# Performance work log

Hardware: AMD Instinct MI355X
Metric: run time of the kernel (lower is better)

The kernel has to match this reference:

```python
import jax, jax.numpy as jnp
import numpy as np


def conv2d(x, w, b, pad=1):
    y = jax.lax.conv_general_dilated(x, w, (1, 1), [(pad, pad), (pad, pad)],
                                     dimension_numbers=('NCHW', 'OIHW', 'NCHW'))
    return y + b[None, :, None, None]


def deform_conv2d(x, offsets, w, b, groups=8, pad=1):
    # torchvision-style deformable conv: offsets [B, 2*G*K, H, W] laid out as
    # (g, k, (dy, dx)); input channels split into G offset groups; zero padding
    # outside the image for bilinear sampling.
    B, C, H, W = x.shape
    kh, kw = w.shape[2], w.shape[3]
    K = kh * kw
    cpg = C // groups
    off = offsets.reshape(B, groups, K, 2, H, W)
    dy, dx = off[:, :, :, 0], off[:, :, :, 1]  # [B,G,K,H,W]
    ky, kx = jnp.meshgrid(jnp.arange(kh), jnp.arange(kw), indexing='ij')
    ky = ky.reshape(K).astype(x.dtype)
    kx = kx.reshape(K).astype(x.dtype)
    ygrid = jnp.arange(H, dtype=x.dtype)
    xgrid = jnp.arange(W, dtype=x.dtype)
    # absolute sampling positions [B,G,K,H,W]
    py = ygrid[None, None, None, :, None] + (ky - pad)[None, None, :, None, None] + dy
    px = xgrid[None, None, None, None, :] + (kx - pad)[None, None, :, None, None] + dx
    y0 = jnp.floor(py)
    x0 = jnp.floor(px)
    wy = py - y0  # frac weights [B,G,K,H,W]
    wx = px - x0
    y0i = y0.astype(jnp.int32)
    x0i = x0.astype(jnp.int32)
    xg = x.reshape(B, groups, cpg, H * W)

    def gather(yc, xc):
        valid = ((yc >= 0) & (yc < H) & (xc >= 0) & (xc < W)).astype(x.dtype)
        idx = jnp.clip(yc, 0, H - 1) * W + jnp.clip(xc, 0, W - 1)
        idx = jnp.broadcast_to(idx.reshape(B, groups, 1, K * H * W),
                               (B, groups, cpg, K * H * W))
        v = jnp.take_along_axis(xg, idx, axis=3).reshape(B, groups, cpg, K, H, W)
        return v * valid[:, :, None]

    v00 = gather(y0i, x0i)
    v01 = gather(y0i, x0i + 1)
    v10 = gather(y0i + 1, x0i)
    v11 = gather(y0i + 1, x0i + 1)
    wy_ = wy[:, :, None]  # [B,G,1,K,H,W]
    wx_ = wx[:, :, None]
    sampled = (v00 * (1 - wy_) * (1 - wx_) + v01 * (1 - wy_) * wx_
               + v10 * wy_ * (1 - wx_) + v11 * wy_ * wx_)
    sampled = sampled.reshape(B, C, K, H, W)
    out = jnp.einsum('bckhw,ock->bohw', sampled, w.reshape(w.shape[0], C, K))
    return out + b[None, :, None, None]


def dab(feat, aux_in, aux_w, aux_b, fw1, fb1, fw2, fb2, se_w1, se_b1, se_w2, se_b2):
    # Adaptive fusion block: project aux (128->64), concat, conv-relu-conv body,
    # SE channel attention (reduction=2), residual add onto feat.
    aux = jax.nn.relu(conv2d(aux_in, aux_w, aux_b))
    x = jnp.concatenate([feat, aux], axis=1)  # [B,128,H,W]
    x = jax.nn.relu(conv2d(x, fw1, fb1))      # 128->64
    x = conv2d(x, fw2, fb2)                   # 64->64
    g = jnp.mean(x, axis=(2, 3))              # [B,64]
    a = jax.nn.sigmoid(jax.nn.relu(g @ se_w1.T + se_b1) @ se_w2.T + se_b2)
    return feat + x * a[:, :, None, None]


def setup_inputs() -> dict:
    key = jax.random.key(0)
    ks = jax.random.split(key, 16)
    B, H, W = 4, 192, 192

    def p(k, shape, s=0.05):
        return jax.random.normal(k, shape, jnp.float32) * s

    return {
        'mv': jax.random.normal(ks[0], (B, 128, H, W), jnp.float32),
        'ref_feature': jax.random.normal(ks[1], (B, 64, H, W), jnp.float32),
        'head_w': p(ks[2], (144, 128, 3, 3)), 'head_b': jnp.zeros((144,), jnp.float32),
        'dcn_w': p(ks[3], (64, 64, 3, 3)), 'dcn_b': jnp.zeros((64,), jnp.float32),
        'c1w1': p(ks[4], (128, 64, 3, 3)), 'c1b1': jnp.zeros((128,), jnp.float32),
        'c1w2': p(ks[5], (128, 128, 3, 3)), 'c1b2': jnp.zeros((128,), jnp.float32),
        'aux_w': p(ks[6], (64, 128, 3, 3)), 'aux_b': jnp.zeros((64,), jnp.float32),
        'fw1': p(ks[7], (64, 128, 3, 3)), 'fb1': jnp.zeros((64,), jnp.float32),
        'fw2': p(ks[8], (64, 64, 3, 3)), 'fb2': jnp.zeros((64,), jnp.float32),
        'se_w1': p(ks[9], (32, 64)), 'se_b1': jnp.zeros((32,), jnp.float32),
        'se_w2': p(ks[10], (64, 32)), 'se_b2': jnp.zeros((64,), jnp.float32),
    }


def reference(mv, ref_feature, head_w, head_b, dcn_w, dcn_b, c1w1, c1b1, c1w2, c1b2,
              aux_w, aux_b, fw1, fb1, fw2, fb2, se_w1, se_b1, se_w2, se_b2):
    offsets = conv2d(mv, head_w, head_b)                       # [B,144,H,W]
    def_feat = jax.nn.relu(deform_conv2d(ref_feature, offsets, dcn_w, dcn_b))
    aux_in = jax.nn.relu(conv2d(jax.nn.relu(conv2d(ref_feature, c1w1, c1b1)),
                                c1w2, c1b2))                   # convs1: 64->128->128
    return dab(def_feat, aux_in, aux_w, aux_b, fw1, fb1, fw2, fb2,
               se_w1, se_b1, se_w2, se_b2)
```

## Files before the change

kernel.cpp:

```cpp
#include <hip/hip_runtime.h>
#include <math.h>

#define HH 192
#define WW 192
#define HWSZ (HH*WW)
#define BB 4

typedef __attribute__((ext_vector_type(8))) short bf16x8;
typedef __attribute__((ext_vector_type(4))) float f32x4;

__device__ __forceinline__ unsigned short f2bf(float f) {
    unsigned int u = __float_as_uint(f);
    u = (u + 0x7FFFu + ((u >> 16) & 1u)) >> 16;
    return (unsigned short)u;
}
__device__ __forceinline__ float bf2f(unsigned short s) {
    return __uint_as_float(((unsigned int)s) << 16);
}

__global__ void prep_all(
    const float* __restrict__ head_w, const float* __restrict__ c1w1,
    const float* __restrict__ c1w2,   const float* __restrict__ aux_w,
    const float* __restrict__ fw1,    const float* __restrict__ fw2,
    const float* __restrict__ dcn_w,
    unsigned short* __restrict__ wb_head, unsigned short* __restrict__ wb_c1w1,
    unsigned short* __restrict__ wb_c1w2, unsigned short* __restrict__ wb_aux,
    unsigned short* __restrict__ wb_fw1,  unsigned short* __restrict__ wb_fw2,
    unsigned short* __restrict__ wdefb2)
{
    int idx = blockIdx.x * 256 + threadIdx.x;
    const float* w; unsigned short* wb; int cout, cin;
    if (idx < 165888)                 { w = head_w; wb = wb_head; cout = 144; cin = 128; }
    else if ((idx -= 165888) < 73728) { w = c1w1;   wb = wb_c1w1; cout = 128; cin = 64;  }
    else if ((idx -= 73728) < 147456) { w = c1w2;   wb = wb_c1w2; cout = 128; cin = 128; }
    else if ((idx -= 147456) < 73728) { w = aux_w;  wb = wb_aux;  cout = 64;  cin = 128; }
    else if ((idx -= 73728) < 73728)  { w = fw1;    wb = wb_fw1;  cout = 64;  cin = 128; }
    else if ((idx -= 73728) < 36864)  { w = fw2;    wb = wb_fw2;  cout = 64;  cin = 64;  }
    else if ((idx -= 36864) < 36864) {
        int o = idx / 576, rem = idx % 576;
        int c = rem / 9, k = rem - c * 9;
        int K = k * 64 + c;
        wdefb2[((size_t)((K >> 5) * 64 + o)) * 32 + (K & 31)] = f2bf(dcn_w[idx]);
        return;
    } else return;
    int o = idx / (cin * 9);
    int rem = idx - o * cin * 9;
    int c = rem / 9;
    int t = rem - c * 9;
    int nch = cin >> 5;
    wb[((t * nch + (c >> 5)) * cout + o) * 32 + (c & 31)] = f2bf(w[idx]);
}

__global__ __launch_bounds__(256) void transpose_all(
    const float* __restrict__ mv, const float* __restrict__ ref,
    unsigned short* __restrict__ mvb, unsigned short* __restrict__ refb,
    unsigned short* __restrict__ refb8)
{
    __shared__ float tile[32][68];
    const int tid = threadIdx.x;
    int bz = blockIdx.z;
    const float* in; unsigned short* outb;
    bool isRef = (bz >= 16);
    int bzr = isRef ? bz - 16 : bz;
    if (isRef) { in = ref; outb = refb; }
    else       { in = mv;  outb = mvb;  }
    const int y = blockIdx.y;
    const int x0 = blockIdx.x * 64;
#pragma unroll
    for (int it = 0; it < 2; ++it) {
        int u = tid + it * 256;
        int c = u >> 4, q = u & 15;
        float4 v = *(const float4*)(in + (((size_t)bzr * 32 + c) * HH + y) * WW + x0 + q * 4);
        *(float4*)&tile[c][q * 4] = v;
    }
    __syncthreads();
    const int pxl = tid >> 2, c8 = tid & 3;
    bf16x8 ov;
#pragma unroll
    for (int j = 0; j < 8; ++j) ov[j] = (short)f2bf(tile[c8 * 8 + j][pxl]);
    *(bf16x8*)(outb + (((size_t)bzr * HH + y) * WW + x0 + pxl) * 32 + c8 * 8) = ov;
    if (isRef) {
        *(bf16x8*)(refb8 + ((size_t)(bzr * 4 + c8) * HWSZ + (size_t)y * WW + x0 + pxl) * 8) = ov;
    }
}

template<int CIN, int COUT_TILE, bool RELU, int EPI>
__global__ __launch_bounds__(256, 3) void conv3x3_v10(
    const unsigned short* __restrict__ in, const unsigned short* __restrict__ wb,
    const float* __restrict__ bias, void* __restrict__ outp,
    int cTot, int ocBase, int nOc, int coutFull, int nPerXcd)
{
    constexpr int NCH = CIN / 32;
    constexpr int NOC = COUT_TILE / 16;
    constexpr int WGR = 36 * COUT_TILE;
    __shared__ __align__(16) unsigned short sx[6 * 72 * 32];
    __shared__ __align__(16) unsigned short sw[288 * COUT_TILE];

    const int tid = threadIdx.x;
    const int d = blockIdx.x;
    const int w = (d & 7) * nPerXcd + (d >> 3);
    const int ocT = (w % nOc) * COUT_TILE;
    int t = w / nOc;
    const int x0 = (t % 3) * 64; t /= 3;
    const int y0 = (t % 48) * 4;
    const int b  = t / 48;
    const int wv = tid >> 6, lane = tid & 63;
    const int l15 = lane & 15, kg = lane >> 4;

    f32x4 acc[NOC][4];
#pragma unroll
    for (int oc = 0; oc < NOC; ++oc)
#pragma unroll
        for (int s = 0; s < 4; ++s) acc[oc][s] = (f32x4){0.f, 0.f, 0.f, 0.f};

    for (int ch = 0; ch < NCH; ++ch) {
#pragma unroll
        for (int it = 0; it < 7; ++it) {
            int u = tid + it * 256;
            if (u < 1728) {
                int r = u / 288;
                int rem = u - r * 288;
                int px = rem >> 2, c8 = rem & 3;
                int yin = y0 - 1 + r;
                int gx  = x0 - 4 + px;
                bf16x8 v = {0,0,0,0,0,0,0,0};
                if (yin >= 0 && yin < HH && gx >= 0 && gx < WW)
                    v = *(const bf16x8*)(in + (((size_t)(b * NCH + ch) * HH + yin) * WW + gx) * 32 + c8 * 8);
                *(bf16x8*)&sx[(r * 72 + px) * 32 + ((c8 ^ ((px >> 1) & 3)) << 3)] = v;
            }
        }
#pragma unroll
        for (int it = 0; it < 7; ++it) {
            int u = tid + it * 256;
            if (u < WGR) {
                int tap = u / (4 * COUT_TILE);
                int rem = u - tap * 4 * COUT_TILE;
                int kgi = rem / COUT_TILE;
                int row = rem - kgi * COUT_TILE;
                bf16x8 v = *(const bf16x8*)(wb
                    + ((size_t)((tap * NCH + ch) * coutFull) + ocT + row) * 32 + kgi * 8);
                *(bf16x8*)&sw[((tap * 4 + kgi) * COUT_TILE + row) * 8] = v;
            }
        }
        __syncthreads();
#pragma unroll
        for (int ky = 0; ky < 3; ++ky) {
#pragma unroll
            for (int kx = 0; kx < 3; ++kx) {
                const int r = wv + ky;
                const int tap = ky * 3 + kx;
                bf16x8 bf[4];
#pragma unroll
                for (int s = 0; s < 4; ++s) {
                    int p = s * 16 + l15 + kx + 3;
                    bf[s] = *(const bf16x8*)&sx[(r * 72 + p) * 32 + ((kg ^ ((p >> 1) & 3)) << 3)];
                }
#pragma unroll
                for (int oc = 0; oc < NOC; ++oc) {
                    bf16x8 a = *(const bf16x8*)&sw[((tap * 4 + kg) * COUT_TILE + oc * 16 + l15) * 8];
#pragma unroll
                    for (int s = 0; s < 4; ++s)
                        acc[oc][s] = __builtin_amdgcn_mfma_f32_16x16x32_bf16(a, bf[s], acc[oc][s], 0, 0, 0);
                }
            }
        }
        __syncthreads();
    }
    const int y = y0 + wv;
    if (EPI == 1) {
        float* out = (float*)outp;
#pragma unroll
        for (int oc = 0; oc < NOC; ++oc)
#pragma unroll
            for (int s = 0; s < 4; ++s) {
                int xo = x0 + s * 16 + l15;
#pragma unroll
                for (int j = 0; j < 4; ++j) {
                    int oL = ocT + oc * 16 + kg * 4 + j;
                    float rv = acc[oc][s][j] + bias[oL];
                    if (RELU) rv = fmaxf(rv, 0.f);
                    out[((size_t)(b * cTot + ocBase + oL) * HH + y) * WW + xo] = rv;
                }
            }
    } else if (EPI == 2) {
        unsigned short* out = (unsigned short*)outp;
#pragma unroll
        for (int oc = 0; oc < NOC; ++oc)
#pragma unroll
            for (int s = 0; s < 4; ++s) {
                int xo = x0 + s * 16 + l15;
#pragma unroll
                for (int j = 0; j < 4; ++j) {
                    int oL = ocT + oc * 16 + kg * 4 + j;
                    float rv = acc[oc][s][j] + bias[oL];
                    if (RELU) rv = fmaxf(rv, 0.f);
                    out[((size_t)(b * cTot + ocBase + oL) * HH + y) * WW + xo] = f2bf(rv);
                }
            }
    } else {
        unsigned short* out = (unsigned short*)outp;
#pragma unroll
        for (int oc = 0; oc < NOC; ++oc) {
            int oL = ocT + oc * 16 + kg * 4;
            int o0 = ocBase + oL;
#pragma unroll
            for (int s = 0; s < 4; ++s) {
                int xo = x0 + s * 16 + l15;
                ushort4 u;
                float r0 = acc[oc][s][0] + bias[oL + 0];
                float r1 = acc[oc][s][1] + bias[oL + 1];
                float r2 = acc[oc][s][2] + bias[oL + 2];
                float r3 = acc[oc][s][3] + bias[oL + 3];
                if (RELU) { r0 = fmaxf(r0,0.f); r1 = fmaxf(r1,0.f); r2 = fmaxf(r2,0.f); r3 = fmaxf(r3,0.f); }
                u.x = f2bf(r0); u.y = f2bf(r1); u.z = f2bf(r2); u.w = f2bf(r3);
                *(ushort4*)(out + ((((size_t)(b * cTot + (o0 >> 5)) * HH + y) * WW + xo) * 32) + (o0 & 31)) = u;
            }
        }
    }
}

__global__ __launch_bounds__(512, 4) void deform_v7(
    const unsigned short* __restrict__ xb8, const unsigned short* __restrict__ offb,
    const unsigned short* __restrict__ wdefb2, const float* __restrict__ bias,
    unsigned short* __restrict__ cat)
{
    __shared__ __align__(16) unsigned short smp[64 * 584];
    const int tid = threadIdx.x;
    const int b = blockIdx.z;
    int flat = blockIdx.x;
    int nf = (flat & 7) * 72 + (flat >> 3);
    const int pixbase = nf * 64;

    const int px = tid & 63, g = tid >> 6;
    const int pix = pixbase + px;
    const int y = pix / WW, x = pix - y * WW;

    const char* xgb = (const char*)(xb8 + (size_t)(b * 8 + g) * HWSZ * 8);
    const unsigned short* ob = offb + ((size_t)(b * 144 + g * 18)) * HWSZ + pix;

    float dyv[9], dxv[9];
#pragma unroll
    for (int k = 0; k < 9; ++k) {
        dyv[k] = bf2f(ob[(size_t)(2 * k) * HWSZ]);
        dxv[k] = bf2f(ob[(size_t)(2 * k + 1) * HWSZ]);
    }

    auto calc = [&](int k, int vo[4], float w4[4]) {
        float pyf = (float)(y + k / 3 - 1) + dyv[k];
        float pxf = (float)(x + k % 3 - 1) + dxv[k];
        float fy = floorf(pyf), fx = floorf(pxf);
        float wy = pyf - fy, wx = pxf - fx;
        int iy = (int)fy, ix = (int)fx;
        float w00 = (1.f - wy) * (1.f - wx), w01 = (1.f - wy) * wx;
        float w10 = wy * (1.f - wx),         w11 = wy * wx;
        bool y0v = (iy >= 0) && (iy < HH);
        bool y1v = (iy + 1 >= 0) && (iy + 1 < HH);
        bool x0v = (ix >= 0) && (ix < WW);
        bool x1v = (ix + 1 >= 0) && (ix + 1 < WW);
        if (!(y0v && x0v)) w00 = 0.f;
        if (!(y0v && x1v)) w01 = 0.f;
        if (!(y1v && x0v)) w10 = 0.f;
        if (!(y1v && x1v)) w11 = 0.f;
        int cy0 = min(max(iy, 0), HH - 1), cy1 = min(max(iy + 1, 0), HH - 1);
        int cx0 = min(max(ix, 0), WW - 1), cx1 = min(max(ix + 1, 0), WW - 1);
        vo[0] = (cy0 * WW + cx0) * 16;
        vo[1] = (cy0 * WW + cx1) * 16;
        vo[2] = (cy1 * WW + cx0) * 16;
        vo[3] = (cy1 * WW + cx1) * 16;
        w4[0] = w00; w4[1] = w01; w4[2] = w10; w4[3] = w11;
    };

    float wr[3][4];
    bf16x8 pf[2][4];
    {
        int vo[4]; calc(0, vo, wr[0]);
#pragma unroll
        for (int j = 0; j < 4; ++j) pf[0][j] = *(const bf16x8*)(xgb + vo[j]);
    }
    {
        int vo[4]; calc(1, vo, wr[1]);
#pragma unroll
        for (int j = 0; j < 4; ++j) pf[1][j] = *(const bf16x8*)(xgb + vo[j]);
    }
    unsigned short* so = smp + px * 584 + g * 8;
#pragma unroll
    for (int k = 0; k < 9; ++k) {
        bf16x8 nx0, nx1, nx2, nx3;
        if (k + 2 < 9) {
            int vo[4]; calc(k + 2, vo, wr[(k + 2) % 3]);
            nx0 = *(const bf16x8*)(xgb + vo[0]);
            nx1 = *(const bf16x8*)(xgb + vo[1]);
            nx2 = *(const bf16x8*)(xgb + vo[2]);
            nx3 = *(const bf16x8*)(xgb + vo[3]);
        }
        __builtin_amdgcn_sched_barrier(0);
        bf16x8 ov;
#pragma unroll
        for (int cc = 0; cc < 8; ++cc) {
            float s = bf2f((unsigned short)pf[k & 1][0][cc]) * wr[k % 3][0]
                    + bf2f((unsigned short)pf[k & 1][1][cc]) * wr[k % 3][1]
                    + bf2f((unsigned short)pf[k & 1][2][cc]) * wr[k % 3][2]
                    + bf2f((unsigned short)pf[k & 1][3][cc]) * wr[k % 3][3];
            ov[cc] = (short)f2bf(s);
        }
        *(bf16x8*)(so + k * 64) = ov;
        if (k + 2 < 9) { pf[k & 1][0] = nx0; pf[k & 1][1] = nx1; pf[k & 1][2] = nx2; pf[k & 1][3] = nx3; }
    }
    __syncthreads();
    const int wv = tid >> 6;
    const int lane = tid & 63, l15 = lane & 15, kg = lane >> 4;
    const int oc = wv >> 1, sp = (wv & 1) * 2;
    f32x4 acc0 = (f32x4){0.f, 0.f, 0.f, 0.f};
    f32x4 acc1 = (f32x4){0.f, 0.f, 0.f, 0.f};
    const unsigned short* arow = wdefb2 + ((size_t)(oc * 16 + l15)) * 32 + kg * 8;
#pragma unroll
    for (int ch = 0; ch < 18; ++ch) {
        bf16x8 b0 = *(const bf16x8*)&smp[(sp * 16 + l15) * 584 + ch * 32 + kg * 8];
        bf16x8 b1 = *(const bf16x8*)&smp[((sp + 1) * 16 + l15) * 584 + ch * 32 + kg * 8];
        bf16x8 a = *(const bf16x8*)(arow + (size_t)ch * 64 * 32);
        acc0 = __builtin_amdgcn_mfma_f32_16x16x32_bf16(a, b0, acc0, 0, 0, 0);
        acc1 = __builtin_amdgcn_mfma_f32_16x16x32_bf16(a, b1, acc1, 0, 0, 0);
    }
    const int o0 = oc * 16 + kg * 4;
#pragma unroll
    for (int s = 0; s < 2; ++s) {
        const f32x4& av = s ? acc1 : acc0;
        int pxo = pixbase + (sp + s) * 16 + l15;
        int yo = pxo / WW, xo = pxo - yo * WW;
        ushort4 u;
        u.x = f2bf(fmaxf(av[0] + bias[o0 + 0], 0.f));
        u.y = f2bf(fmaxf(av[1] + bias[o0 + 1], 0.f));
        u.z = f2bf(fmaxf(av[2] + bias[o0 + 2], 0.f));
        u.w = f2bf(fmaxf(av[3] + bias[o0 + 3], 0.f));
        *(ushort4*)(cat + ((((size_t)(b * 4 + (o0 >> 5)) * HH + yo) * WW + xo) * 32) + (o0 & 31)) = u;
    }
}

__global__ __launch_bounds__(256) void pool_kernel(const float* __restrict__ x, float* __restrict__ gout)
{
    int bc = blockIdx.x;
    const float* p = x + (size_t)bc * HWSZ;
    int tid = threadIdx.x;
    float s = 0.f;
    for (int i = tid * 4; i < HWSZ; i += 256 * 4) {
        float4 v = *reinterpret_cast<const float4*>(p + i);
        s += v.x + v.y + v.z + v.w;
    }
#pragma unroll
    for (int o = 32; o > 0; o >>= 1) s += __shfl_down(s, o, 64);
    __shared__ float red[4];
    if ((tid & 63) == 0) red[tid >> 6] = s;
    __syncthreads();
    if (tid == 0) gout[bc] = (red[0] + red[1] + red[2] + red[3]) * (1.f / (float)HWSZ);
}

__global__ __launch_bounds__(256) void se_kernel(
    const float* __restrict__ g, const float* __restrict__ w1, const float* __restrict__ b1,
    const float* __restrict__ w2, const float* __restrict__ b2, float* __restrict__ a)
{
    __shared__ float sg[BB * 64];
    __shared__ float sh[BB * 32];
    int tid = threadIdx.x;
    sg[tid] = g[tid];
    __syncthreads();
    if (tid < BB * 32) {
        int b = tid / 32, h = tid % 32;
        float s = b1[h];
        for (int c = 0; c < 64; ++c) s += sg[b * 64 + c] * w1[h * 64 + c];
        sh[b * 32 + h] = fmaxf(s, 0.f);
    }
    __syncthreads();
    {
        int b = tid / 64, o = tid % 64;
        float s = b2[o];
        for (int h = 0; h < 32; ++h) s += sh[b * 32 + h] * w2[o * 32 + h];
        a[tid] = 1.f / (1.f + expf(-s));
    }
}

__global__ __launch_bounds__(256) void final_v2(
    float* __restrict__ out, const unsigned short* __restrict__ catb, const float* __restrict__ a)
{
    const int VPC = HWSZ / 4;
    int v = blockIdx.x * 256 + threadIdx.x;
    int bc = v / VPC, within = v - bc * VPC;
    int b = bc >> 6, c = bc & 63;
    float av = a[bc];
    int pix = within * 4;
    int y = pix / WW, x = pix - y * WW;
    const unsigned short* dbase = catb
        + (((size_t)(b * 4 + (c >> 5)) * HH + y) * WW + x) * 32 + (c & 31);
    float4 xo = reinterpret_cast<float4*>(out)[v];
    float4 r;
    r.x = bf2f(dbase[0])  + xo.x * av;
    r.y = bf2f(dbase[32]) + xo.y * av;
    r.z = bf2f(dbase[64]) + xo.z * av;
    r.w = bf2f(dbase[96]) + xo.w * av;
    reinterpret_cast<float4*>(out)[v] = r;
}

extern "C" void kernel_launch(void* const* d_in, const int* in_sizes, int n_in,
                              void* d_out, int out_size, void* d_ws, size_t ws_size,
                              hipStream_t stream) {
    const float* mv     = (const float*)d_in[0];
    const float* ref    = (const float*)d_in[1];
    const float* head_w = (const float*)d_in[2];
    const float* head_b = (const float*)d_in[3];
    const float* dcn_w  = (const float*)d_in[4];
    const float* dcn_b  = (const float*)d_in[5];
    const float* c1w1   = (const float*)d_in[6];
    const float* c1b1   = (const float*)d_in[7];
    const float* c1w2   = (const float*)d_in[8];
    const float* c1b2   = (const float*)d_in[9];
    const float* aux_w  = (const float*)d_in[10];
    const float* aux_b  = (const float*)d_in[11];
    const float* fw1    = (const float*)d_in[12];
    const float* fb1    = (const float*)d_in[13];
    const float* fw2    = (const float*)d_in[14];
    const float* fb2    = (const float*)d_in[15];
    const float* se_w1  = (const float*)d_in[16];
    const float* se_b1  = (const float*)d_in[17];
    const float* se_w2  = (const float*)d_in[18];
    const float* se_b2  = (const float*)d_in[19];
    float* out = (float*)d_out;

    float* ws = (float*)d_ws;
    unsigned short* offb     = (unsigned short*)ws;
    unsigned short* mvb      = (unsigned short*)(ws + 21233664);
    unsigned short* refb     = (unsigned short*)(ws + 30670848);
    unsigned short* catb     = (unsigned short*)(ws + 35389440);
    unsigned short* r2b      = (unsigned short*)(ws + 44826624);
    unsigned short* wdefb2   = (unsigned short*)(ws + 54263808);
    unsigned short* wbb      = (unsigned short*)(ws + 54282240);
    unsigned short* refb8    = wbb + 571392;
    float* gbuf              = (float*)(refb8 + 9437184 + 16);
    float* abuf              = gbuf + 256;
    unsigned short* t1b      = (unsigned short*)ws;

    unsigned short* wb_head = wbb;
    unsigned short* wb_c1w1 = wb_head + 165888;
    unsigned short* wb_c1w2 = wb_c1w1 + 73728;
    unsigned short* wb_aux  = wb_c1w2 + 147456;
    unsigned short* wb_fw1  = wb_aux  + 73728;
    unsigned short* wb_fw2  = wb_fw1  + 73728;

    prep_all<<<2376, 256, 0, stream>>>(head_w, c1w1, c1w2, aux_w, fw1, fw2, dcn_w,
                                       wb_head, wb_c1w1, wb_c1w2, wb_aux, wb_fw1, wb_fw2, wdefb2);
    transpose_all<<<dim3(3, 192, 24), 256, 0, stream>>>(mv, ref, mvb, refb, refb8);

    conv3x3_v10<128, 48, false, 2><<<1728, 256, 0, stream>>>(
        mvb, wb_head, head_b, offb, 144, 0, 3, 144, 216);
    deform_v7<<<dim3(576, 1, BB), 512, 0, stream>>>(refb8, offb, wdefb2, dcn_b, catb);
    conv3x3_v10<64, 32, true, 0><<<2304, 256, 0, stream>>>(
        refb, wb_c1w1, c1b1, t1b, 4, 0, 4, 128, 288);
    conv3x3_v10<128, 32, true, 0><<<2304, 256, 0, stream>>>(
        t1b, wb_c1w2, c1b2, r2b, 4, 0, 4, 128, 288);
    conv3x3_v10<128, 32, true, 0><<<1152, 256, 0, stream>>>(
        r2b, wb_aux, aux_b, catb, 4, 64, 2, 64, 144);
    conv3x3_v10<128, 32, true, 0><<<1152, 256, 0, stream>>>(
        catb, wb_fw1, fb1, r2b, 2, 0, 2, 64, 144);
    conv3x3_v10<64, 32, false, 1><<<1152, 256, 0, stream>>>(
        r2b, wb_fw2, fb2, out, 64, 0, 2, 64, 144);
    pool_kernel<<<BB * 64, 256, 0, stream>>>(out, gbuf);
    se_kernel<<<1, 256, 0, stream>>>(gbuf, se_w1, se_b1, se_w2, se_b2, abuf);
    final_v2<<<9216, 256, 0, stream>>>(out, catb, abuf);
}
```

Before: 435.0 us.

## Keep last conv output in bf16 channel-blocked layout for pooling and final fuse

The final 3x3 conv now writes bf16 in the 32-channel-blocked layout into a reused workspace buffer, instead of fp32 NCHW into the output. A new pooling kernel reduces that bf16 buffer per 32-channel block, and the final SE-scale-plus-residual kernel reads it instead of re-reading fp32 output. The aim is to cut the fp32 write and two fp32 reads of the intermediate. In exchange, the pre-SE activations are rounded to bf16, and pooling now runs on only 8 blocks, which may underuse the GPU.

Measured after the change: 601.5 us. 38.3% more time.

```diff
diff --git a/kernel.cpp b/kernel.cpp
--- a/kernel.cpp
+++ b/kernel.cpp
@@ -336,22 +336,30 @@
     }
 }
 
-__global__ __launch_bounds__(256) void pool_kernel(const float* __restrict__ x, float* __restrict__ gout)
-{
-    int bc = blockIdx.x;
-    const float* p = x + (size_t)bc * HWSZ;
-    int tid = threadIdx.x;
-    float s = 0.f;
-    for (int i = tid * 4; i < HWSZ; i += 256 * 4) {
-        float4 v = *reinterpret_cast<const float4*>(p + i);
-        s += v.x + v.y + v.z + v.w;
-    }
-#pragma unroll
-    for (int o = 32; o > 0; o >>= 1) s += __shfl_down(s, o, 64);
-    __shared__ float red[4];
-    if ((tid & 63) == 0) red[tid >> 6] = s;
+__global__ __launch_bounds__(256) void pool_cl32(
+    const unsigned short* __restrict__ x2b, float* __restrict__ gout)
+{
+    __shared__ float red[256][8];
+    const int blk = blockIdx.x;
+    const unsigned short* base = x2b + (size_t)blk * HWSZ * 32;
+    const int tid = threadIdx.x;
+    const int c8 = tid & 3, pg = tid >> 2;
+    float acc[8];
+#pragma unroll
+    for (int j = 0; j < 8; ++j) acc[j] = 0.f;
+    for (int p = pg; p < HWSZ; p += 64) {
+        bf16x8 v = *(const bf16x8*)(base + (size_t)p * 32 + c8 * 8);
+#pragma unroll
+        for (int j = 0; j < 8; ++j) acc[j] += bf2f((unsigned short)v[j]);
+    }
+#pragma unroll
+    for (int j = 0; j < 8; ++j) red[tid][j] = acc[j];
     __syncthreads();
-    if (tid == 0) gout[bc] = (red[0] + red[1] + red[2] + red[3]) * (1.f / (float)HWSZ);
+    if (tid < 32) {
+        float s = 0.f;
+        for (int j = 0; j < 64; ++j) s += red[(j << 2) | (tid >> 3)][tid & 7];
+        gout[(blk >> 1) * 64 + (blk & 1) * 32 + tid] = s * (1.f / (float)HWSZ);
+    }
 }
 
 __global__ __launch_bounds__(256) void se_kernel(
@@ -378,8 +386,9 @@
     }
 }
 
-__global__ __launch_bounds__(256) void final_v2(
-    float* __restrict__ out, const unsigned short* __restrict__ catb, const float* __restrict__ a)
+__global__ __launch_bounds__(256) void final_v3(
+    float* __restrict__ out, const unsigned short* __restrict__ catb,
+    const unsigned short* __restrict__ x2b, const float* __restrict__ a)
 {
     const int VPC = HWSZ / 4;
     int v = blockIdx.x * 256 + threadIdx.x;
@@ -390,12 +399,13 @@
     int y = pix / WW, x = pix - y * WW;
     const unsigned short* dbase = catb
         + (((size_t)(b * 4 + (c >> 5)) * HH + y) * WW + x) * 32 + (c & 31);
-    float4 xo = reinterpret_cast<float4*>(out)[v];
+    const unsigned short* xbase = x2b
+        + (((size_t)(b * 2 + (c >> 5)) * HH + y) * WW + x) * 32 + (c & 31);
     float4 r;
-    r.x = bf2f(dbase[0])  + xo.x * av;
-    r.y = bf2f(dbase[32]) + xo.y * av;
-    r.z = bf2f(dbase[64]) + xo.z * av;
-    r.w = bf2f(dbase[96]) + xo.w * av;
+    r.x = bf2f(dbase[0])  + bf2f(xbase[0])  * av;
+    r.y = bf2f(dbase[32]) + bf2f(xbase[32]) * av;
+    r.z = bf2f(dbase[64]) + bf2f(xbase[64]) * av;
+    r.w = bf2f(dbase[96]) + bf2f(xbase[96]) * av;
     reinterpret_cast<float4*>(out)[v] = r;
 }
 
@@ -436,6 +446,7 @@
     float* gbuf              = (float*)(refb8 + 9437184 + 16);
     float* abuf              = gbuf + 256;
     unsigned short* t1b      = (unsigned short*)ws;
+    unsigned short* x2b      = mvb;
 
     unsigned short* wb_head = wbb;
     unsigned short* wb_c1w1 = wb_head + 165888;
@@ -459,9 +470,9 @@
         r2b, wb_aux, aux_b, catb, 4, 64, 2, 64, 144);
     conv3x3_v10<128, 32, true, 0><<<1152, 256, 0, stream>>>(
         catb, wb_fw1, fb1, r2b, 2, 0, 2, 64, 144);
-    conv3x3_v10<64, 32, false, 1><<<1152, 256, 0, stream>>>(
-        r2b, wb_fw2, fb2, out, 64, 0, 2, 64, 144);
-    pool_kernel<<<BB * 64, 256, 0, stream>>>(out, gbuf);
+    conv3x3_v10<64, 32, false, 0><<<1152, 256, 0, stream>>>(
+        r2b, wb_fw2, fb2, x2b, 2, 0, 2, 64, 144);
+    pool_cl32<<<BB * 2, 256, 0, stream>>>(x2b, gbuf);
     se_kernel<<<1, 256, 0, stream>>>(gbuf, se_w1, se_b1, se_w2, se_b2, abuf);
-    final_v2<<<9216, 256, 0, stream>>>(out, catb, abuf);
-}
+    final_v3<<<9216, 256, 0, stream>>>(out, catb, x2b, abuf);
+}
```
